# Performance work log

Hardware: AMD Instinct MI355X
Metric: run time of the kernel (lower is better)

Reference implementation:

```python
import jax, jax.numpy as jnp
import numpy as np

N = 8192
D_IN = 256
D_HID = 256
D_OUT = 256


def setup_inputs() -> dict:
    key = jax.random.key(0)
    k_x, k_a, k_q, k_k, k_v = jax.random.split(key, 5)
    X = jax.random.normal(k_x, (N, D_IN), dtype=jnp.float32)
    # binary adjacency, zero diagonal (module adds self-loops via +eye)
    A = jax.random.randint(k_a, (N, N), 0, 2, dtype=jnp.int32)
    A = A * (1 - jnp.eye(N, dtype=jnp.int32))
    # parameters: randn / 10, as in the torch __init__
    Wq = jax.random.normal(k_q, (D_IN, D_HID), dtype=jnp.float32) / 10.0
    Wk = jax.random.normal(k_k, (D_IN, D_HID), dtype=jnp.float32) / 10.0
    Wv = jax.random.normal(k_v, (D_IN, D_OUT), dtype=jnp.float32) / 10.0
    return {"X": X, "A": A, "Wq": Wq, "Wk": Wk, "Wv": Wv}


def reference(X, A, Wq, Wk, Wv):
    n = A.shape[0]
    Af = A.astype(X.dtype) + jnp.eye(n, dtype=X.dtype)  # add self-loops
    Q = X @ Wq  # [N, H]
    K = X @ Wk  # [N, H]
    V = X @ Wv  # [N, O]
    S = Q @ K.T  # [N, N]
    # torch: nan_to_num(-inf*(1-A), nan=0) -> 0 where A==1, finite-min where A==0
    mask = jnp.nan_to_num(-jnp.inf * (1.0 - Af), nan=0.0)
    P = jax.nn.softmax(S + mask, axis=1)
    return P @ V  # [N, O]
```

## Files before the change

### kernel.cpp

```cpp
#include <hip/hip_runtime.h>
#include <stdint.h>


typedef _Float16 f16;
typedef unsigned short u16;
typedef __attribute__((ext_vector_type(8))) _Float16 f16x8;
typedef __attribute__((ext_vector_type(4))) _Float16 f16x4;
typedef __attribute__((ext_vector_type(4))) float f32x4;

#define NN 8192
#define DD 256
#define BR 128
#define BC 64
#define CCH 4
#define COLS (NN / CCH)
#define NIT (COLS / BC)
#define PSTR 80

#define MFMA(a, b, c) __builtin_amdgcn_mfma_f32_16x16x32_f16((a), (b), (c), 0, 0, 0)

__device__ __forceinline__ void gl2lds16(const void* g, void* l) {
    __builtin_amdgcn_global_load_lds(
        (const __attribute__((address_space(1))) unsigned int*)g,
        (__attribute__((address_space(3))) unsigned int*)l, 16, 0, 0);
}

__device__ __forceinline__ u16 f16bits(f16 h) {
    union { f16 h; u16 u; } c;
    c.h = h;
    return c.u;
}

__global__ void splitX_kernel(const float4* __restrict__ X, f16x4* __restrict__ Xh,
                              f16x4* __restrict__ Xl) {
    const int i = blockIdx.x * blockDim.x + threadIdx.x;
    const float4 v = X[i];
    const f16 h0 = (f16)v.x, h1 = (f16)v.y, h2 = (f16)v.z, h3 = (f16)v.w;
    f16x4 H = {h0, h1, h2, h3};
    f16x4 L = {(f16)(v.x - (float)h0), (f16)(v.y - (float)h1), (f16)(v.z - (float)h2),
               (f16)(v.w - (float)h3)};
    Xh[i] = H;
    Xl[i] = L;
}

__global__ void splitW_kernel(const float* __restrict__ Wq, const float* __restrict__ Wk,
                              const float* __restrict__ Wv, f16* __restrict__ WtH,
                              f16* __restrict__ WtL) {
    const int i = blockIdx.x * blockDim.x + threadIdx.x;
    const int mat = i >> 16;
    const int k = (i >> 8) & 255;
    const int n = i & 255;
    const float* W = (mat == 0) ? Wq : ((mat == 1) ? Wk : Wv);
    const float v = W[k * 256 + n];
    const f16 h = (f16)v;
    const size_t o = (size_t)(mat * 256 + n) * 256 + k;
    WtH[o] = h;
    WtL[o] = (f16)(v - (float)h);
}

__global__ __launch_bounds__(256, 2) void qkv_kernel(
    const f16* __restrict__ Xh, const f16* __restrict__ Xl,
    const f16* __restrict__ WtH, const f16* __restrict__ WtL,
    f16* __restrict__ Qh, f16* __restrict__ Ql,
    f16* __restrict__ Kh, f16* __restrict__ Vt) {
    __shared__ f16 Wh[64 * 256];
    __shared__ f16 Wl[64 * 256];
    const int lane = threadIdx.x & 63;
    const int w = threadIdx.x >> 6;
    const int l15 = lane & 15;
    const int quad = lane >> 4;
    const int r0 = blockIdx.x * 64;
    const int mat = blockIdx.y;

    f16x8 xh[8], xl[8];
    const size_t xb = (size_t)(r0 + w * 16 + l15) * DD + quad * 8;
#pragma unroll
    for (int kc = 0; kc < 8; ++kc) {
        xh[kc] = *(const f16x8*)(Xh + xb + kc * 32);
        xl[kc] = *(const f16x8*)(Xl + xb + kc * 32);
    }
    const int orow = r0 + w * 16 + quad * 4;

#pragma unroll 1
    for (int c = 0; c < 4; ++c) {
        const int nb = mat * 256 + c * 64;
#pragma unroll
        for (int i = 0; i < 8; ++i) {
            const int r = w * 16 + i * 2 + (lane >> 5);
            gl2lds16(WtH + (size_t)(nb + r) * DD + (((lane & 31) ^ (r & 7)) * 8),
                     &Wh[(w * 16 + i * 2) * 256]);
        }
#pragma unroll
        for (int i = 0; i < 8; ++i) {
            const int r = w * 16 + i * 2 + (lane >> 5);
            gl2lds16(WtL + (size_t)(nb + r) * DD + (((lane & 31) ^ (r & 7)) * 8),
                     &Wl[(w * 16 + i * 2) * 256]);
        }
        __syncthreads();

        const f32x4 fzero = {0.f, 0.f, 0.f, 0.f};
        f32x4 acc[4];
#pragma unroll
        for (int nt = 0; nt < 4; ++nt) acc[nt] = fzero;
#pragma unroll
        for (int kc = 0; kc < 8; ++kc)
#pragma unroll
            for (int nt = 0; nt < 4; ++nt) {
                const int r = nt * 16 + l15;
                const int blk = (((kc * 4 + quad) ^ (r & 7)) * 8);
                const f16x8 wh = *(const f16x8*)&Wh[r * 256 + blk];
                const f16x8 wl = *(const f16x8*)&Wl[r * 256 + blk];
                acc[nt] = MFMA(xh[kc], wh, acc[nt]);
                acc[nt] = MFMA(xh[kc], wl, acc[nt]);
                acc[nt] = MFMA(xl[kc], wh, acc[nt]);
            }

        if (mat == 0) {
#pragma unroll
            for (int nt = 0; nt < 4; ++nt)
#pragma unroll
                for (int rg = 0; rg < 4; ++rg) {
                    const int col = c * 64 + nt * 16 + l15;
                    const float v = acc[nt][rg];
                    const f16 h = (f16)v;
                    Qh[(size_t)(orow + rg) * DD + col] = h;
                    Ql[(size_t)(orow + rg) * DD + col] = (f16)(v - (float)h);
                }
        } else if (mat == 1) {
#pragma unroll
            for (int nt = 0; nt < 4; ++nt)
#pragma unroll
                for (int rg = 0; rg < 4; ++rg) {
                    const int col = c * 64 + nt * 16 + l15;
                    Kh[(size_t)(orow + rg) * DD + col] = (f16)acc[nt][rg];
                }
        } else {
#pragma unroll
            for (int nt = 0; nt < 4; ++nt) {
                const int n = c * 64 + nt * 16 + l15;
                ushort4 pk;
                pk.x = f16bits((f16)acc[nt][0]);
                pk.y = f16bits((f16)acc[nt][1]);
                pk.z = f16bits((f16)acc[nt][2]);
                pk.w = f16bits((f16)acc[nt][3]);
                *(ushort4*)(Vt + (size_t)n * NN + orow) = pk;
            }
        }
        __syncthreads();
    }
}

__global__ __launch_bounds__(512, 2) void flash_kernel(
    const f16* __restrict__ Qh, const f16* __restrict__ Ql,
    const f16* __restrict__ Kh, const f16* __restrict__ Vt,
    const int* __restrict__ A,
    float* __restrict__ pO, float* __restrict__ pM, float* __restrict__ pL) {
    __shared__ f16 Klds[2][64 * 256];
    __shared__ f16 Vlds[2][256 * 64];
    __shared__ f16 Plds[8][16 * PSTR];

    const int lane = threadIdx.x & 63;
    const int w = threadIdx.x >> 6;
    const int l15 = lane & 15;
    const int quad = lane >> 4;
    const int bid = blockIdx.x;
    const int cch = bid & 3;
    const int r0 = (bid >> 2) * BR;
    const int col0 = cch * COLS;

    f16x8 qh[8], ql[8];
    {
        const size_t qb = (size_t)(r0 + w * 16 + l15) * DD + quad * 8;
#pragma unroll
        for (int kc = 0; kc < 8; ++kc) {
            qh[kc] = *(const f16x8*)(Qh + qb + kc * 32);
            ql[kc] = *(const f16x8*)(Ql + qb + kc * 32);
        }
    }

    const f32x4 fzero = {0.f, 0.f, 0.f, 0.f};
    f32x4 accO[16];
#pragma unroll
    for (int i = 0; i < 16; ++i) accO[i] = fzero;
    float mrow[4], lpart[4];
#pragma unroll
    for (int r = 0; r < 4; ++r) {
        mrow[r] = -1e30f;
        lpart[r] = 0.f;
    }
    const int growb = r0 + w * 16 + quad * 4;
    f16* Pw = &Plds[w][0];

    auto stage = [&](int t, int b) {
        const int j0 = col0 + t * BC;
#pragma unroll
        for (int i = 0; i < 4; ++i) {
            const int r = w * 8 + i * 2 + (lane >> 5);
            gl2lds16(Kh + (size_t)(j0 + r) * DD + (((lane & 31) ^ (r & 7)) * 8),
                     &Klds[b][(w * 8 + i * 2) * 256]);
        }
#pragma unroll
        for (int i = 0; i < 4; ++i) {
            const int n = w * 32 + i * 8 + (lane >> 3);
            gl2lds16(Vt + (size_t)n * NN + j0 + (((lane & 7) ^ (n & 7)) * 8),
                     &Vlds[b][(w * 32 + i * 8) * 64]);
        }
    };

    stage(0, 0);
    __syncthreads();

#pragma unroll 1
    for (int it = 0; it < NIT; ++it) {
        const int cur = it & 1;
        const int j0 = col0 + it * BC;

        if (it + 1 < NIT) stage(it + 1, cur ^ 1);

        int av[4][4];
#pragma unroll
        for (int rgi = 0; rgi < 4; ++rgi)
#pragma unroll
            for (int jt = 0; jt < 4; ++jt)
                av[rgi][jt] = __builtin_nontemporal_load(
                    A + (size_t)(growb + rgi) * NN + j0 + jt * 16 + l15);

        f32x4 accS[4];
#pragma unroll
        for (int jt = 0; jt < 4; ++jt) accS[jt] = fzero;
#pragma unroll
        for (int kc = 0; kc < 8; ++kc)
#pragma unroll
            for (int jt = 0; jt < 4; ++jt) {
                const int r = jt * 16 + l15;
                const f16x8 kf =
                    *(const f16x8*)&Klds[cur][r * 256 + (((kc * 4 + quad) ^ (r & 7)) * 8)];
                accS[jt] = MFMA(qh[kc], kf, accS[jt]);
                accS[jt] = MFMA(ql[kc], kf, accS[jt]);
            }

        float alpha[4];
#pragma unroll
        for (int rgi = 0; rgi < 4; ++rgi) {
            const int gr = growb + rgi;
            float mx = -3.0e38f;
#pragma unroll
            for (int jt = 0; jt < 4; ++jt) {
                const int gc = j0 + jt * 16 + l15;
                const float s = (av[rgi][jt] != 0 || gr == gc) ? accS[jt][rgi] : -3.0e38f;
                accS[jt][rgi] = s;
                mx = fmaxf(mx, s);
            }
#pragma unroll
            for (int off = 1; off < 16; off <<= 1) mx = fmaxf(mx, __shfl_xor(mx, off, 64));
            const float mnew = fmaxf(mrow[rgi], mx);
            alpha[rgi] = __expf(mrow[rgi] - mnew);
            mrow[rgi] = mnew;
            float rs = 0.f;
#pragma unroll
            for (int jt = 0; jt < 4; ++jt) {
                const float s = accS[jt][rgi];
                const float e = (s > -1.0e37f) ? __expf(s - mnew) : 0.f;
                rs += e;
                Pw[(quad * 4 + rgi) * PSTR + jt * 16 + l15] = (f16)e;
            }
            lpart[rgi] = lpart[rgi] * alpha[rgi] + rs;
        }
#pragma unroll
        for (int nt = 0; nt < 16; ++nt)
#pragma unroll
            for (int rgi = 0; rgi < 4; ++rgi) accO[nt][rgi] *= alpha[rgi];

        f16x8 pf[2];
        pf[0] = *(const f16x8*)&Pw[l15 * PSTR + quad * 8];
        pf[1] = *(const f16x8*)&Pw[l15 * PSTR + 32 + quad * 8];

#pragma unroll
        for (int nt = 0; nt < 16; ++nt)
#pragma unroll
            for (int kc2 = 0; kc2 < 2; ++kc2) {
                const int n = nt * 16 + l15;
                const f16x8 vf =
                    *(const f16x8*)&Vlds[cur][n * 64 + (((kc2 * 4 + quad) ^ (n & 7)) * 8)];
                accO[nt] = MFMA(pf[kc2], vf, accO[nt]);
            }

        __syncthreads();
    }

#pragma unroll
    for (int rgi = 0; rgi < 4; ++rgi)
#pragma unroll
        for (int off = 1; off < 16; off <<= 1)
            lpart[rgi] += __shfl_xor(lpart[rgi], off, 64);

#pragma unroll
    for (int nt = 0; nt < 16; ++nt)
#pragma unroll
        for (int rgi = 0; rgi < 4; ++rgi)
            pO[((size_t)cch * NN + growb + rgi) * DD + nt * 16 + l15] = accO[nt][rgi];
    if (l15 == 0) {
#pragma unroll
        for (int rgi = 0; rgi < 4; ++rgi) {
            pM[(size_t)cch * NN + growb + rgi] = mrow[rgi];
            pL[(size_t)cch * NN + growb + rgi] = lpart[rgi];
        }
    }
}

__global__ __launch_bounds__(256) void merge_kernel(const float* __restrict__ pO,
                                                    const float* __restrict__ pM,
                                                    const float* __restrict__ pL,
                                                    float* __restrict__ out) {
    const int n = threadIdx.x;
#pragma unroll 1
    for (int rr = 0; rr < 8; ++rr) {
        const int row = blockIdx.x * 8 + rr;
        float mc[CCH], lc[CCH];
        float M = -3e38f;
#pragma unroll
        for (int c = 0; c < CCH; ++c) {
            mc[c] = pM[(size_t)c * NN + row];
            lc[c] = pL[(size_t)c * NN + row];
            M = fmaxf(M, mc[c]);
        }
        float L = 0.f, acc = 0.f;
#pragma unroll
        for (int c = 0; c < CCH; ++c) {
            const float wgt = __expf(mc[c] - M);
            L += wgt * lc[c];
            acc += wgt * pO[((size_t)c * NN + row) * DD + n];
        }
        out[(size_t)row * DD + n] = acc / L;
    }
}

extern "C" void kernel_launch(void* const* d_in, const int* in_sizes, int n_in,
                              void* d_out, int out_size, void* d_ws, size_t ws_size,
                              hipStream_t stream) {
    const float* X = (const float*)d_in[0];
    const int* A = (const int*)d_in[1];
    const float* Wq = (const float*)d_in[2];
    const float* Wk = (const float*)d_in[3];
    const float* Wv = (const float*)d_in[4];
    float* out = (float*)d_out;

    char* ws = (char*)d_ws;
    const size_t MB = 1ull << 20;
    f16* Xh = (f16*)(ws + 0 * MB);
    f16* Xl = (f16*)(ws + 4 * MB);
    f16* WtH = (f16*)(ws + 8 * MB);
    f16* WtL = (f16*)(ws + 8 * MB + 512 * 1024);
    f16* Qh = (f16*)(ws + 9 * MB);
    f16* Ql = (f16*)(ws + 13 * MB);
    f16* Kh = (f16*)(ws + 17 * MB);
    f16* Vt = (f16*)(ws + 21 * MB);
    float* pO = (float*)(ws + 25 * MB);
    float* pM = (float*)(ws + 57 * MB);
    float* pL = (float*)(ws + 57 * MB + 256 * 1024);
    (void)ws_size; (void)in_sizes; (void)n_in; (void)out_size;

    splitX_kernel<<<2048, 256, 0, stream>>>((const float4*)X, (f16x4*)Xh, (f16x4*)Xl);
    splitW_kernel<<<768, 256, 0, stream>>>(Wq, Wk, Wv, WtH, WtL);
    qkv_kernel<<<dim3(NN / 64, 3), 256, 0, stream>>>(Xh, Xl, WtH, WtL, Qh, Ql, Kh, Vt);
    flash_kernel<<<(NN / BR) * CCH, 512, 0, stream>>>(Qh, Ql, Kh, Vt, A, pO, pM, pL);
    merge_kernel<<<NN / 8, 256, 0, stream>>>(pO, pM, pL, out);
}
```

Before: 496.2 us.

## Single-buffer K/V LDS, double column chunks, store partial outputs in fp16

Removes LDS double buffering of K and V tiles so shared memory per block drops, and raises launch bounds to four blocks per CU. Doubles the column split to eight chunks for more blocks, writes partial O in fp16 to halve merge traffic, and replaces padded P staging with an XOR-swizzled layout. The trade is that each tile load is no longer overlapped with compute and must be followed by a barrier, the tighter launch bound may force register spills with 16 accumulator vectors plus Q fragments, and the fp16 partials lose precision.

```diff
diff --git a/kernel.cpp b/kernel.cpp
--- a/kernel.cpp
+++ b/kernel.cpp
@@ -12,10 +12,9 @@
 #define DD 256
 #define BR 128
 #define BC 64
-#define CCH 4
+#define CCH 8
 #define COLS (NN / CCH)
 #define NIT (COLS / BC)
-#define PSTR 80
 
 #define MFMA(a, b, c) __builtin_amdgcn_mfma_f32_16x16x32_f16((a), (b), (c), 0, 0, 0)
 
@@ -30,6 +29,8 @@
     c.h = h;
     return c.u;
 }
+
+__device__ __forceinline__ int pswz(int row) { return (row ^ (row >> 2)) & 7; }
 
 __global__ void splitX_kernel(const float4* __restrict__ X, f16x4* __restrict__ Xh,
                               f16x4* __restrict__ Xl) {
@@ -150,22 +151,22 @@
     }
 }
 
-__global__ __launch_bounds__(512, 2) void flash_kernel(
+__global__ __launch_bounds__(512, 4) void flash_kernel(
     const f16* __restrict__ Qh, const f16* __restrict__ Ql,
     const f16* __restrict__ Kh, const f16* __restrict__ Vt,
     const int* __restrict__ A,
-    float* __restrict__ pO, float* __restrict__ pM, float* __restrict__ pL) {
-    __shared__ f16 Klds[2][64 * 256];
-    __shared__ f16 Vlds[2][256 * 64];
-    __shared__ f16 Plds[8][16 * PSTR];
+    f16* __restrict__ pO, float* __restrict__ pM, float* __restrict__ pL) {
+    __shared__ f16 Klds[64 * 256];
+    __shared__ f16 Vlds[256 * 64];
+    __shared__ f16 Plds[8][16 * 64];
 
     const int lane = threadIdx.x & 63;
     const int w = threadIdx.x >> 6;
     const int l15 = lane & 15;
     const int quad = lane >> 4;
     const int bid = blockIdx.x;
-    const int cch = bid & 3;
-    const int r0 = (bid >> 2) * BR;
+    const int cch = bid & 7;
+    const int r0 = (bid >> 3) * BR;
     const int col0 = cch * COLS;
 
     f16x8 qh[8], ql[8];
@@ -191,31 +192,22 @@
     const int growb = r0 + w * 16 + quad * 4;
     f16* Pw = &Plds[w][0];
 
-    auto stage = [&](int t, int b) {
-        const int j0 = col0 + t * BC;
+#pragma unroll 1
+    for (int it = 0; it < NIT; ++it) {
+        const int j0 = col0 + it * BC;
+
 #pragma unroll
         for (int i = 0; i < 4; ++i) {
             const int r = w * 8 + i * 2 + (lane >> 5);
             gl2lds16(Kh + (size_t)(j0 + r) * DD + (((lane & 31) ^ (r & 7)) * 8),
-                     &Klds[b][(w * 8 + i * 2) * 256]);
+                     &Klds[(w * 8 + i * 2) * 256]);
         }
 #pragma unroll
         for (int i = 0; i < 4; ++i) {
             const int n = w * 32 + i * 8 + (lane >> 3);
             gl2lds16(Vt + (size_t)n * NN + j0 + (((lane & 7) ^ (n & 7)) * 8),
-                     &Vlds[b][(w * 32 + i * 8) * 64]);
-        }
-    };
-
-    stage(0, 0);
-    __syncthreads();
-
-#pragma unroll 1
-    for (int it = 0; it < NIT; ++it) {
-        const int cur = it & 1;
-        const int j0 = col0 + it * BC;
-
-        if (it + 1 < NIT) stage(it + 1, cur ^ 1);
+                     &Vlds[(w * 32 + i * 8) * 64]);
+        }
 
         int av[4][4];
 #pragma unroll
@@ -225,6 +217,8 @@
                 av[rgi][jt] = __builtin_nontemporal_load(
                     A + (size_t)(growb + rgi) * NN + j0 + jt * 16 + l15);
 
+        __syncthreads();
+
         f32x4 accS[4];
 #pragma unroll
         for (int jt = 0; jt < 4; ++jt) accS[jt] = fzero;
@@ -234,7 +228,7 @@
             for (int jt = 0; jt < 4; ++jt) {
                 const int r = jt * 16 + l15;
                 const f16x8 kf =
-                    *(const f16x8*)&Klds[cur][r * 256 + (((kc * 4 + quad) ^ (r & 7)) * 8)];
+                    *(const f16x8*)&Klds[r * 256 + (((kc * 4 + quad) ^ (r & 7)) * 8)];
                 accS[jt] = MFMA(qh[kc], kf, accS[jt]);
                 accS[jt] = MFMA(ql[kc], kf, accS[jt]);
             }
@@ -257,12 +251,14 @@
             alpha[rgi] = __expf(mrow[rgi] - mnew);
             mrow[rgi] = mnew;
             float rs = 0.f;
+            const int lrow = quad * 4 + rgi;
 #pragma unroll
             for (int jt = 0; jt < 4; ++jt) {
                 const float s = accS[jt][rgi];
                 const float e = (s > -1.0e37f) ? __expf(s - mnew) : 0.f;
                 rs += e;
-                Pw[(quad * 4 + rgi) * PSTR + jt * 16 + l15] = (f16)e;
+                const int col = jt * 16 + l15;
+                Pw[lrow * 64 + (((col >> 3) ^ pswz(lrow)) * 8) + (col & 7)] = (f16)e;
             }
             lpart[rgi] = lpart[rgi] * alpha[rgi] + rs;
         }
@@ -272,8 +268,8 @@
             for (int rgi = 0; rgi < 4; ++rgi) accO[nt][rgi] *= alpha[rgi];
 
         f16x8 pf[2];
-        pf[0] = *(const f16x8*)&Pw[l15 * PSTR + quad * 8];
-        pf[1] = *(const f16x8*)&Pw[l15 * PSTR + 32 + quad * 8];
+        pf[0] = *(const f16x8*)&Pw[l15 * 64 + (((0 * 4 + quad) ^ pswz(l15)) * 8)];
+        pf[1] = *(const f16x8*)&Pw[l15 * 64 + (((1 * 4 + quad) ^ pswz(l15)) * 8)];
 
 #pragma unroll
         for (int nt = 0; nt < 16; ++nt)
@@ -281,7 +277,7 @@
             for (int kc2 = 0; kc2 < 2; ++kc2) {
                 const int n = nt * 16 + l15;
                 const f16x8 vf =
-                    *(const f16x8*)&Vlds[cur][n * 64 + (((kc2 * 4 + quad) ^ (n & 7)) * 8)];
+                    *(const f16x8*)&Vlds[n * 64 + (((kc2 * 4 + quad) ^ (n & 7)) * 8)];
                 accO[nt] = MFMA(pf[kc2], vf, accO[nt]);
             }
 
@@ -298,7 +294,8 @@
     for (int nt = 0; nt < 16; ++nt)
 #pragma unroll
         for (int rgi = 0; rgi < 4; ++rgi)
-            pO[((size_t)cch * NN + growb + rgi) * DD + nt * 16 + l15] = accO[nt][rgi];
+            pO[((size_t)cch * NN + growb + rgi) * DD + nt * 16 + l15] =
+                (f16)accO[nt][rgi];
     if (l15 == 0) {
 #pragma unroll
         for (int rgi = 0; rgi < 4; ++rgi) {
@@ -308,7 +305,7 @@
     }
 }
 
-__global__ __launch_bounds__(256) void merge_kernel(const float* __restrict__ pO,
+__global__ __launch_bounds__(256) void merge_kernel(const f16* __restrict__ pO,
                                                     const float* __restrict__ pM,
                                                     const float* __restrict__ pL,
                                                     float* __restrict__ out) {
@@ -329,7 +326,7 @@
         for (int c = 0; c < CCH; ++c) {
             const float wgt = __expf(mc[c] - M);
             L += wgt * lc[c];
-            acc += wgt * pO[((size_t)c * NN + row) * DD + n];
+            acc += wgt * (float)pO[((size_t)c * NN + row) * DD + n];
         }
         out[(size_t)row * DD + n] = acc / L;
     }
@@ -355,7 +352,7 @@
     f16* Ql = (f16*)(ws + 13 * MB);
     f16* Kh = (f16*)(ws + 17 * MB);
     f16* Vt = (f16*)(ws + 21 * MB);
-    float* pO = (float*)(ws + 25 * MB);
+    f16* pO = (f16*)(ws + 25 * MB);
     float* pM = (float*)(ws + 57 * MB);
     float* pL = (float*)(ws + 57 * MB + 256 * 1024);
     (void)ws_size; (void)in_sizes; (void)n_in; (void)out_size;
```

Result: slower. 768.8 us (+54.9%).
